# Kernel tuning notes

Measured on AMD Instinct MI355X. Metric: run time of the kernel, lower is better.

## Reference

```python
import jax, jax.numpy as jnp
import numpy as np


def setup_inputs() -> dict:
    key = jax.random.key(0)
    ks = jax.random.split(key, 5)
    B, T, C, HS = 8, 2048, 1024, 64
    return {
        "x_q": jax.random.normal(ks[0], (B, T, C), dtype=jnp.float32),
        "x_kv": jax.random.normal(ks[1], (B, T, C), dtype=jnp.float32),
        "Wq": jax.random.normal(ks[2], (C, HS), dtype=jnp.float32) * (C ** -0.5),
        "Wk": jax.random.normal(ks[3], (C, HS), dtype=jnp.float32) * (C ** -0.5),
        "Wv": jax.random.normal(ks[4], (C, HS), dtype=jnp.float32) * (C ** -0.5),
    }


def reference(x_q, x_kv, Wq, Wk, Wv):
    # x_q, x_kv: [B, T, C]; W*: [C, HS]
    B, T, C = x_q.shape
    q = jnp.einsum("btc,ch->bth", x_q, Wq)   # [B, T, HS]
    k = jnp.einsum("btc,ch->bth", x_kv, Wk)  # [B, T, HS]
    v = jnp.einsum("btc,ch->bth", x_kv, Wv)  # [B, T, HS]
    # NOTE: original scales by d_model**-0.5 (C), not head_size**-0.5
    wei = jnp.einsum("bqh,bkh->bqk", q, k) * (C ** -0.5)  # [B, T, T]
    causal = jnp.tril(jnp.ones((T, T), dtype=bool))
    wei = jnp.where(causal, wei, -jnp.inf)
    wei = jax.nn.softmax(wei, axis=-1)
    out = jnp.einsum("bqk,bkh->bqh", wei, v)  # [B, T, HS]
    return out
```

## Files before the change

### kernel.cpp

```cpp
#include <hip/hip_runtime.h>

typedef __bf16 bf16_t;
typedef __bf16 bf16x8 __attribute__((ext_vector_type(8)));
typedef float f32x4 __attribute__((ext_vector_type(4)));
typedef unsigned short u16x4 __attribute__((ext_vector_type(4)));

#define B_ 8
#define T_ 2048
#define C_ 1024
#define HS_ 64
#define VSTRIDE 2080

#define MFMA __builtin_amdgcn_mfma_f32_16x16x32_bf16

__device__ __forceinline__ float fast_exp2(float x) {
#if __has_builtin(__builtin_amdgcn_exp2f)
  return __builtin_amdgcn_exp2f(x);
#else
  return exp2f(x);
#endif
}

__device__ __forceinline__ void async_ld16(const void* gsrc, void* lds_dst) {
  __builtin_amdgcn_global_load_lds(
      (const __attribute__((address_space(1))) void*)gsrc,
      (__attribute__((address_space(3))) void*)lds_dst, 16, 0, 0);
}

__global__ __launch_bounds__(256) void repack_w(
    const float* __restrict__ Wq, const float* __restrict__ Wk,
    const float* __restrict__ Wv, bf16_t* __restrict__ pq,
    bf16_t* __restrict__ pk, bf16_t* __restrict__ pv) {
  const float* W = (blockIdx.y == 0) ? Wq : ((blockIdx.y == 1) ? Wk : Wv);
  bf16_t* P = (blockIdx.y == 0) ? pq : ((blockIdx.y == 1) ? pk : pv);
  int t = blockIdx.x * 256 + threadIdx.x;
  int lane = t & 63, nt = (t >> 6) & 3, kc = t >> 8;
  int quad = lane >> 4, ln = lane & 15;
  bf16x8 v;
#pragma unroll
  for (int j = 0; j < 8; ++j)
    v[j] = (bf16_t)W[(kc * 32 + quad * 8 + j) * HS_ + nt * 16 + ln];
  *(bf16x8*)(P + (size_t)t * 8) = v;
}

__global__ __launch_bounds__(512, 2) void proj_mfma(
    const float* __restrict__ xq, const float* __restrict__ xkv,
    const bf16_t* __restrict__ pq, const bf16_t* __restrict__ pk,
    const bf16_t* __restrict__ pv, bf16_t* __restrict__ q,
    bf16_t* __restrict__ k, bf16_t* __restrict__ vT) {
  __shared__ float Xb[2][16][1028];
  __shared__ float red[2][4][4][16][4];

  const bool is_kv = (blockIdx.y != 0);
  const float* x = is_kv ? xkv : xq;

  const int w = threadIdx.x >> 6, lane = threadIdx.x & 63;
  const int quad = lane >> 4, ln = lane & 15;
  const int kh = w >> 2, nt = w & 3;

  bf16x8 bfr[32];
#pragma unroll
  for (int j = 0; j < 16; ++j) {
    const size_t idx = (((size_t)(kh * 16 + j) * 4 + nt) * 64 + lane) * 8;
    bfr[j * 2] = *(const bf16x8*)((is_kv ? pk : pq) + idx);
    if (is_kv) bfr[j * 2 + 1] = *(const bf16x8*)(pv + idx);
  }

  auto STAGE = [&](int c) {
    const size_t g = (size_t)blockIdx.x * 8 + c;
    const int buf = c & 1;
#pragma unroll
    for (int i = 0; i < 2; ++i) {
      const int r = w * 2 + i;
      const float* src = x + (g * 16 + r) * C_;
#pragma unroll
      for (int qt = 0; qt < 4; ++qt)
        async_ld16(src + qt * 256 + lane * 4, &Xb[buf][r][qt * 256]);
    }
  };

  auto COMPUTE = [&](int buf, f32x4& a0, f32x4& a1) {
    const char* rp = (const char*)&Xb[buf][ln][0];
    if (is_kv) {
#pragma unroll
      for (int j = 0; j < 16; ++j) {
        const int s0 = (kh * 16 + j) * 8 + quad * 2;
        f32x4 xlo = *(const f32x4*)(rp + s0 * 16);
        f32x4 xhi = *(const f32x4*)(rp + s0 * 16 + 16);
        bf16x8 a;
#pragma unroll
        for (int jj = 0; jj < 4; ++jj) {
          a[jj] = (bf16_t)xlo[jj];
          a[4 + jj] = (bf16_t)xhi[jj];
        }
        a0 = MFMA(a, bfr[j * 2], a0, 0, 0, 0);
        a1 = MFMA(a, bfr[j * 2 + 1], a1, 0, 0, 0);
      }
    } else {
#pragma unroll
      for (int j = 0; j < 16; ++j) {
        const int s0 = (kh * 16 + j) * 8 + quad * 2;
        f32x4 xlo = *(const f32x4*)(rp + s0 * 16);
        f32x4 xhi = *(const f32x4*)(rp + s0 * 16 + 16);
        bf16x8 a;
#pragma unroll
        for (int jj = 0; jj < 4; ++jj) {
          a[jj] = (bf16_t)xlo[jj];
          a[4 + jj] = (bf16_t)xhi[jj];
        }
        a0 = MFMA(a, bfr[j * 2], a0, 0, 0, 0);
      }
    }
  };

  u16x4 ow0[8], ow1[8];

  STAGE(0);
  STAGE(1);
  asm volatile("s_waitcnt vmcnt(8)" ::: "memory");
  __builtin_amdgcn_s_barrier();
  __builtin_amdgcn_sched_barrier(0);

#pragma unroll
  for (int c = 0; c < 8; ++c) {
    f32x4 acc0 = (f32x4){0.f, 0.f, 0.f, 0.f};
    f32x4 acc1 = (f32x4){0.f, 0.f, 0.f, 0.f};
    COMPUTE(c & 1, acc0, acc1);
    if (kh == 1) {
      *(f32x4*)&red[0][nt][quad][ln][0] = acc0;
      if (is_kv) *(f32x4*)&red[1][nt][quad][ln][0] = acc1;
    }
    asm volatile("s_waitcnt lgkmcnt(0)" ::: "memory");
    __builtin_amdgcn_s_barrier();
    __builtin_amdgcn_sched_barrier(0);
    if (kh == 0) {
      acc0 += *(const f32x4*)&red[0][nt][quad][ln][0];
      if (is_kv) acc1 += *(const f32x4*)&red[1][nt][quad][ln][0];
#pragma unroll
      for (int r = 0; r < 4; ++r) {
        bf16_t h0 = (bf16_t)acc0[r];
        ow0[c][r] = *(unsigned short*)&h0;
        bf16_t h1 = (bf16_t)acc1[r];
        ow1[c][r] = *(unsigned short*)&h1;
      }
    }
    if (c == 7) break;
    if (c < 6) {
      STAGE(c + 2);
      asm volatile("s_waitcnt vmcnt(8)" ::: "memory");
    } else {
      asm volatile("s_waitcnt vmcnt(0)" ::: "memory");
    }
    __builtin_amdgcn_s_barrier();
    __builtin_amdgcn_sched_barrier(0);
  }

  if (kh != 0) return;
  if (!is_kv) {
#pragma unroll
    for (int c = 0; c < 8; ++c) {
      const int R0 = (blockIdx.x * 8 + c) * 16;
#pragma unroll
      for (int r = 0; r < 4; ++r)
        *((unsigned short*)q + (size_t)(R0 + quad * 4 + r) * HS_ + nt * 16 +
          ln) = ow0[c][r];
    }
  } else {
#pragma unroll
    for (int c = 0; c < 8; ++c) {
      const int R0 = (blockIdx.x * 8 + c) * 16;
#pragma unroll
      for (int r = 0; r < 4; ++r)
        *((unsigned short*)k + (size_t)(R0 + quad * 4 + r) * HS_ + nt * 16 +
          ln) = ow0[c][r];
      const int bb = R0 >> 11;
      const int t0 = (R0 & (T_ - 1)) + quad * 4;
      *(u16x4*)((unsigned short*)vT +
                ((size_t)(bb * HS_ + nt * 16 + ln)) * VSTRIDE + t0) = ow1[c];
    }
  }
}

__global__ __launch_bounds__(512, 4) void attn_mfma(
    const bf16_t* __restrict__ q, const bf16_t* __restrict__ k,
    const bf16_t* __restrict__ vT, float* __restrict__ out) {
  __shared__ bf16_t p_lds[8][16][80];
  __shared__ float o_buf[8][16][66];
  __shared__ float l_buf[8][16][17];

  const int b = blockIdx.x & 7;
  const int gq = 127 - (blockIdx.x >> 3);
  const int w = threadIdx.x >> 6, lane = threadIdx.x & 63;
  const int quad = lane >> 4, ln = lane & 15;
  const int qr0 = gq * 16;
  const size_t bt = (size_t)b * T_;
  const int td = gq >> 2;

  bf16x8 aq[2];
#pragma unroll
  for (int hc = 0; hc < 2; ++hc)
    aq[hc] = *(const bf16x8*)(q + (bt + qr0 + ln) * HS_ + hc * 32 + quad * 8);

  f32x4 o_acc[4];
  float l_part[4] = {0.f, 0.f, 0.f, 0.f};
#pragma unroll
  for (int nt = 0; nt < 4; ++nt) o_acc[nt] = (f32x4){0.f, 0.f, 0.f, 0.f};
  const float scl = 0.03125f * 1.44269504088896340736f;

  bf16x8 bk[8], bv[8];
  int t = w;
  if (t <= td) {
#pragma unroll
    for (int hc = 0; hc < 2; ++hc)
#pragma unroll
      for (int nt = 0; nt < 4; ++nt)
        bk[hc * 4 + nt] = *(const bf16x8*)(k + (bt + t * 64 + nt * 16 + ln) * HS_ +
                                           hc * 32 + quad * 8);
  }

  for (; t <= td; t += 8) {
    const int kr0 = t * 64;

#pragma unroll
    for (int kc = 0; kc < 2; ++kc)
#pragma unroll
      for (int nt = 0; nt < 4; ++nt)
        bv[kc * 4 + nt] = *(const bf16x8*)(vT +
                                           ((size_t)(b * HS_ + nt * 16 + ln)) * VSTRIDE +
                                           kr0 + kc * 32 + quad * 8);

    f32x4 s[4];
#pragma unroll
    for (int nt = 0; nt < 4; ++nt) s[nt] = (f32x4){0.f, 0.f, 0.f, 0.f};
#pragma unroll
    for (int hc = 0; hc < 2; ++hc)
#pragma unroll
      for (int nt = 0; nt < 4; ++nt)
        s[nt] = MFMA(aq[hc], bk[hc * 4 + nt], s[nt], 0, 0, 0);

    if (t + 8 <= td) {
#pragma unroll
      for (int hc = 0; hc < 2; ++hc)
#pragma unroll
        for (int nt = 0; nt < 4; ++nt)
          bk[hc * 4 + nt] = *(const bf16x8*)(k +
                                             (bt + (t + 8) * 64 + nt * 16 + ln) * HS_ +
                                             hc * 32 + quad * 8);
    }

    const bool diag = (t == td);
#pragma unroll
    for (int nt = 0; nt < 4; ++nt)
#pragma unroll
      for (int r = 0; r < 4; ++r) {
        float e = fast_exp2(s[nt][r] * scl);
        if (diag && (kr0 + nt * 16 + ln > qr0 + quad * 4 + r)) e = 0.f;
        l_part[r] += e;
        p_lds[w][quad * 4 + r][nt * 16 + ln] = (bf16_t)e;
      }

#pragma unroll
    for (int kc = 0; kc < 2; ++kc) {
      bf16x8 ap = *(const bf16x8*)&p_lds[w][ln][kc * 32 + quad * 8];
#pragma unroll
      for (int nt = 0; nt < 4; ++nt)
        o_acc[nt] = MFMA(ap, bv[kc * 4 + nt], o_acc[nt], 0, 0, 0);
    }
  }

#pragma unroll
  for (int nt = 0; nt < 4; ++nt)
#pragma unroll
    for (int r = 0; r < 4; ++r)
      o_buf[w][quad * 4 + r][nt * 16 + ln] = o_acc[nt][r];
#pragma unroll
  for (int r = 0; r < 4; ++r) l_buf[w][quad * 4 + r][ln] = l_part[r];
  __syncthreads();

#pragma unroll
  for (int rr = 0; rr < 2; ++rr) {
    const int row = w + rr * 8;
    float o = 0.f, lsum = 0.f;
#pragma unroll
    for (int ww = 0; ww < 8; ++ww) {
      o += o_buf[ww][row][lane];
      lsum += l_buf[ww][row][lane & 15];
    }
#pragma unroll
    for (int off = 1; off < 16; off <<= 1) lsum += __shfl_xor(lsum, off);
    out[(bt + qr0 + row) * HS_ + lane] = o / lsum;
  }
}

extern "C" void kernel_launch(void* const* d_in, const int* in_sizes, int n_in,
                              void* d_out, int out_size, void* d_ws,
                              size_t ws_size, hipStream_t stream) {
  (void)in_sizes; (void)n_in; (void)out_size; (void)ws_size;
  const float* xq = (const float*)d_in[0];
  const float* xkv = (const float*)d_in[1];
  const float* Wq = (const float*)d_in[2];
  const float* Wk = (const float*)d_in[3];
  const float* Wv = (const float*)d_in[4];
  float* out = (float*)d_out;

  char* ws = (char*)d_ws;
  bf16_t* q = (bf16_t*)ws;
  bf16_t* kk = (bf16_t*)(ws + (2u << 20));
  bf16_t* vT = (bf16_t*)(ws + (4u << 20));
  bf16_t* pq = (bf16_t*)(ws + (6656u << 10));
  bf16_t* pk = (bf16_t*)(ws + (6784u << 10));
  bf16_t* pv = (bf16_t*)(ws + (6912u << 10));

  repack_w<<<dim3(32, 3), 256, 0, stream>>>(Wq, Wk, Wv, pq, pk, pv);
  proj_mfma<<<dim3(128, 2), 512, 0, stream>>>(xq, xkv, pq, pk, pv, q, kk, vT);
  attn_mfma<<<dim3(1024), 512, 0, stream>>>(q, kk, vT, out);
}
```

Before: 197.3 us.

## Stage projection inputs through registers instead of direct global-to-LDS loads

The projection kernel's X staging changes from direct global-to-LDS async loads to a register-staged pipeline. Each step issues global loads for chunk c+2 into registers, while the registers holding chunk c+1 are written to LDS after waiting on vmcnt. Scheduling barriers are also added after the K/V prefetch loads in the attention kernel so the loads issue early. This trades the LDS-DMA path for extra VGPRs and explicit ds_write instructions, with a full vmcnt(0) wait at each step that may reduce memory overlap.

```diff
diff --git a/kernel.cpp b/kernel.cpp
--- a/kernel.cpp
+++ b/kernel.cpp
@@ -19,12 +19,6 @@
 #else
   return exp2f(x);
 #endif
-}
-
-__device__ __forceinline__ void async_ld16(const void* gsrc, void* lds_dst) {
-  __builtin_amdgcn_global_load_lds(
-      (const __attribute__((address_space(1))) void*)gsrc,
-      (__attribute__((address_space(3))) void*)lds_dst, 16, 0, 0);
 }
 
 __global__ __launch_bounds__(256) void repack_w(
@@ -66,16 +60,22 @@
     if (is_kv) bfr[j * 2 + 1] = *(const bf16x8*)(pv + idx);
   }
 
-  auto STAGE = [&](int c) {
+  f32x4 R[8];
+  auto ISSUE = [&](int c) {
     const size_t g = (size_t)blockIdx.x * 8 + c;
+#pragma unroll
+    for (int i = 0; i < 8; ++i) {
+      const int r = w * 2 + (i >> 2);
+      R[i] = *(const f32x4*)(x + (g * 16 + r) * C_ + (i & 3) * 256 + lane * 4);
+    }
+    __builtin_amdgcn_sched_barrier(0);
+  };
+  auto WRITE = [&](int c) {
     const int buf = c & 1;
 #pragma unroll
-    for (int i = 0; i < 2; ++i) {
-      const int r = w * 2 + i;
-      const float* src = x + (g * 16 + r) * C_;
-#pragma unroll
-      for (int qt = 0; qt < 4; ++qt)
-        async_ld16(src + qt * 256 + lane * 4, &Xb[buf][r][qt * 256]);
+    for (int i = 0; i < 8; ++i) {
+      const int r = w * 2 + (i >> 2);
+      *(f32x4*)&Xb[buf][r][(i & 3) * 256 + lane * 4] = R[i];
     }
   };
 
@@ -115,9 +115,11 @@
 
   u16x4 ow0[8], ow1[8];
 
-  STAGE(0);
-  STAGE(1);
-  asm volatile("s_waitcnt vmcnt(8)" ::: "memory");
+  ISSUE(0);
+  asm volatile("s_waitcnt vmcnt(0)" ::: "memory");
+  WRITE(0);
+  ISSUE(1);
+  asm volatile("s_waitcnt lgkmcnt(0)" ::: "memory");
   __builtin_amdgcn_s_barrier();
   __builtin_amdgcn_sched_barrier(0);
 
@@ -145,12 +147,10 @@
       }
     }
     if (c == 7) break;
-    if (c < 6) {
-      STAGE(c + 2);
-      asm volatile("s_waitcnt vmcnt(8)" ::: "memory");
-    } else {
-      asm volatile("s_waitcnt vmcnt(0)" ::: "memory");
-    }
+    asm volatile("s_waitcnt vmcnt(0)" ::: "memory");
+    WRITE(c + 1);
+    if (c + 2 < 8) ISSUE(c + 2);
+    asm volatile("s_waitcnt lgkmcnt(0)" ::: "memory");
     __builtin_amdgcn_s_barrier();
     __builtin_amdgcn_sched_barrier(0);
   }
@@ -216,6 +216,7 @@
       for (int nt = 0; nt < 4; ++nt)
         bk[hc * 4 + nt] = *(const bf16x8*)(k + (bt + t * 64 + nt * 16 + ln) * HS_ +
                                            hc * 32 + quad * 8);
+    __builtin_amdgcn_sched_barrier(0);
   }
 
   for (; t <= td; t += 8) {
@@ -228,6 +229,7 @@
         bv[kc * 4 + nt] = *(const bf16x8*)(vT +
                                            ((size_t)(b * HS_ + nt * 16 + ln)) * VSTRIDE +
                                            kr0 + kc * 32 + quad * 8);
+    __builtin_amdgcn_sched_barrier(0);
 
     f32x4 s[4];
 #pragma unroll
@@ -246,6 +248,7 @@
           bk[hc * 4 + nt] = *(const bf16x8*)(k +
                                              (bt + (t + 8) * 64 + nt * 16 + ln) * HS_ +
                                              hc * 32 + quad * 8);
+      __builtin_amdgcn_sched_barrier(0);
     }
 
     const bool diag = (t == td);
```

Result: no change. 194.7 us (-1.4%).
